# Kernel optimization log

Measured on AMD Instinct MI355X. Metric: run time of the kernel, lower is better.

Reference implementation:

```python
import jax, jax.numpy as jnp
import numpy as np

N_SPK = 8      # MAX_NO_OF_SPEAKERS
N_LAYERS = 2


def setup_inputs() -> dict:
    key = jax.random.key(0)
    B, S, H = 8, 1024, 512  # batch, seq_len, input_size==hidden_size==output_size
    k = jax.random.split(key, 6)
    x = jax.random.normal(k[0], (B, S, H), dtype=jnp.float32)
    speakers = jax.random.randint(k[1], (B, S), 0, N_SPK, dtype=jnp.int32)
    scale = 1.0 / np.sqrt(H).astype(np.float32)
    # per-speaker, per-layer GRU params (torch nn.GRU layout: gates [r,z,n])
    Wi = jax.random.uniform(k[2], (N_SPK, N_LAYERS, 3 * H, H), minval=-scale, maxval=scale, dtype=jnp.float32)
    Wh = jax.random.uniform(k[3], (N_SPK, N_LAYERS, 3 * H, H), minval=-scale, maxval=scale, dtype=jnp.float32)
    bi = jax.random.uniform(k[4], (N_SPK, N_LAYERS, 3 * H), minval=-scale, maxval=scale, dtype=jnp.float32)
    bh = jax.random.uniform(k[5], (N_SPK, N_LAYERS, 3 * H), minval=-scale, maxval=scale, dtype=jnp.float32)
    return {"x": x, "speakers": speakers, "Wi": Wi, "Wh": Wh, "bi": bi, "bh": bh}


def _gru_cell(x_t, h, Wi_l, Wh_l, bi_l, bh_l):
    # torch GRU cell: r,z,n gates
    gi = x_t @ Wi_l.T + bi_l          # [B, 3H]
    gh = h @ Wh_l.T + bh_l            # [B, 3H]
    ir, iz, i_n = jnp.split(gi, 3, axis=-1)
    hr, hz, h_n = jnp.split(gh, 3, axis=-1)
    r = jax.nn.sigmoid(ir + hr)
    z = jax.nn.sigmoid(iz + hz)
    n = jnp.tanh(i_n + r * h_n)
    return (1.0 - z) * n + z * h


def _forward(x, speakers, Wi, Wh, bi, bh):
    B, S, H = x.shape
    x_sb = jnp.swapaxes(x, 0, 1)              # [S, B, H]
    total = jnp.zeros((S, B, H), x.dtype)
    for sp in range(N_SPK):
        # masked-GRU equivalence: gathering speaker sp's utterances, running a
        # GRU, and scattering back == running over the full sequence while
        # freezing hidden state (and emitting 0) at non-sp timesteps.
        mask_sb = (speakers == sp).T          # [S, B]
        Wi_s, Wh_s, bi_s, bh_s = Wi[sp], Wh[sp], bi[sp], bh[sp]

        def step(h, xm):
            x_t, m_t = xm                     # [B,H], [B]
            m = m_t[:, None]
            inp = x_t
            new_h = []
            for l in range(N_LAYERS):
                hl = _gru_cell(inp, h[l], Wi_s[l], Wh_s[l], bi_s[l], bh_s[l])
                hl = jnp.where(m, hl, h[l])   # carry hidden across masked steps
                new_h.append(hl)
                inp = hl
            return jnp.stack(new_h), jnp.where(m, inp, 0.0)

        h0 = jnp.zeros((N_LAYERS, B, H), x.dtype)
        _, outs = jax.lax.scan(step, h0, (x_sb, mask_sb))  # outs: [S, B, H]
        total = total + outs                  # masks disjoint across speakers
    return jnp.swapaxes(total, 0, 1)          # [B, S, H]


def reference(x, speakers, Wi, Wh, bi, bh):
    return _forward(x, speakers, Wi, Wh, bi, bh)
```

## Files before the change

### kernel.cpp

```cpp
#include <hip/hip_runtime.h>
#include <cstdint>
#include <cstddef>

#define SS 1024
#define HH 512
#define G3 1536

typedef _Float16 half8 __attribute__((ext_vector_type(8)));
typedef float f32x4 __attribute__((ext_vector_type(4)));

static constexpr unsigned OFF_TLIST = 0;
static constexpr unsigned OFF_LEN   = 262144;
static constexpr unsigned OFF_META  = 262400;
static constexpr unsigned OFF_H0    = 262656;
static constexpr unsigned OFF_H1    = OFF_H0 + 131072;
static constexpr unsigned OFF_BAR   = OFF_H1 + 131072;
static constexpr unsigned WS_NEED   = OFF_BAR + 4096;

__device__ __forceinline__ half8 cvt8(const float* p) {
  float4 u = *(const float4*)p;
  float4 v = *(const float4*)(p + 4);
  half8 h;
  h[0]=(_Float16)u.x; h[1]=(_Float16)u.y; h[2]=(_Float16)u.z; h[3]=(_Float16)u.w;
  h[4]=(_Float16)v.x; h[5]=(_Float16)v.y; h[6]=(_Float16)v.z; h[7]=(_Float16)v.w;
  return h;
}

__device__ __forceinline__ float sigm(float x) { return 1.f / (1.f + __expf(-x)); }

__global__ void prep_kernel(const int* __restrict__ spk, int* __restrict__ tlist,
                            int* __restrict__ len, int* __restrict__ meta) {
  __shared__ int slen[64];
  const int t = threadIdx.x;
  const int sp = t >> 3, b = t & 7;
  int cnt = 0;
  int* tl = tlist + (sp * 8 + b) * SS;
  const int4* srow = (const int4*)(spk + b * SS);
#pragma unroll 4
  for (int i = 0; i < SS / 4; ++i) {
    int4 v = srow[i];
    if (v.x == sp) tl[cnt++] = 4 * i + 0;
    if (v.y == sp) tl[cnt++] = 4 * i + 1;
    if (v.z == sp) tl[cnt++] = 4 * i + 2;
    if (v.w == sp) tl[cnt++] = 4 * i + 3;
  }
  len[t] = cnt;
  slen[t] = cnt;
  for (int i = cnt; i < SS; ++i) tl[i] = 0;
  __syncthreads();
  if (t < 8) {
    int m = 0;
    for (int i = 0; i < 8; ++i) m = max(m, slen[t * 8 + i]);
    meta[t] = m;
  }
}

__launch_bounds__(256, 1)
__global__ void gru_main(const float* __restrict__ x,
                         const float* __restrict__ Wi, const float* __restrict__ Wh,
                         const float* __restrict__ bi, const float* __restrict__ bh,
                         const int* __restrict__ tlist, const int* __restrict__ len,
                         const int* __restrict__ meta,
                         unsigned short* __restrict__ h0ring,
                         unsigned short* __restrict__ h1ring,
                         float* __restrict__ out, unsigned* __restrict__ bar) {
  const int wg = blockIdx.x;
  const int sp = wg & 7;
  const int og = wg >> 3;
  const int j0 = og * 16;
  const int tid = threadIdx.x;
  const int w  = tid >> 6;
  const int l  = tid & 63;
  const int lr = l & 15;
  const int lg = l >> 4;
  const int b8 = lr & 7;

  __shared__ float accbuf[4][12][272];
  __shared__ _Float16 hstage[2][8][536];

  const size_t WMAT = (size_t)G3 * HH;
  const float* pWi0 = Wi + (size_t)(sp * 2 + 0) * WMAT;
  const float* pWh0 = Wh + (size_t)(sp * 2 + 0) * WMAT;
  const float* pWi1 = Wi + (size_t)(sp * 2 + 1) * WMAT;
  const float* pWh1 = Wh + (size_t)(sp * 2 + 1) * WMAT;

  half8 bwi0[3][4], bwh0[3][4], bwi1[3][4], bwh1[3][4];
#pragma unroll
  for (int T = 0; T < 3; ++T) {
#pragma unroll
    for (int q = 0; q < 4; ++q) {
      const size_t row = (size_t)(T * HH + j0 + lr);
      const int k0 = lg * 8 + (w * 4 + q) * 32;
      bwi0[T][q] = cvt8(pWi0 + row * HH + k0);
      bwh0[T][q] = cvt8(pWh0 + row * HH + k0);
      bwi1[T][q] = cvt8(pWi1 + row * HH + k0);
      bwh1[T][q] = cvt8(pWh1 + row * HH + k0);
    }
  }

  const bool isA = tid < 128;
  const int u_ = isA ? tid : (tid - 128);
  const int gb = u_ >> 4;
  const int gj = u_ & 15;
  const int Lb = len[sp * 8 + gb];
  const int* tlB = tlist + (sp * 8 + gb) * SS;
  float bAi[3], bAh[3], bBi[3], bBh[3];
#pragma unroll
  for (int g = 0; g < 3; ++g) {
    const int n = g * HH + j0 + gj;
    bAi[g] = bi[(sp * 2 + 0) * G3 + n];
    bAh[g] = bh[(sp * 2 + 0) * G3 + n];
    bBi[g] = bi[(sp * 2 + 1) * G3 + n];
    bBh[g] = bh[(sp * 2 + 1) * G3 + n];
  }

  const int* tlX = tlist + (sp * 8 + b8) * SS;
  const float* xrow_base = x + (size_t)b8 * SS * HH;

  const int maxlen = meta[sp];
  unsigned* flg = bar + sp * 32;

  float h0prev = 0.f, h1prev = 0.f;

  {
    const int tx = tlX[0];
    const float* xs = xrow_base + (size_t)tx * HH;
    half8 xf[4];
    f32x4 a0[3];
#pragma unroll
    for (int T = 0; T < 3; ++T)
#pragma unroll
      for (int e = 0; e < 4; ++e) a0[T][e] = 0.f;
#pragma unroll
    for (int q = 0; q < 4; ++q) xf[q] = cvt8(xs + lg * 8 + (w * 4 + q) * 32);
#pragma unroll
    for (int T = 0; T < 3; ++T)
#pragma unroll
      for (int q = 0; q < 4; ++q)
        a0[T] = __builtin_amdgcn_mfma_f32_16x16x32_f16(xf[q], bwi0[T][q], a0[T], 0, 0, 0);
#pragma unroll
    for (int T = 0; T < 3; ++T)
#pragma unroll
      for (int e = 0; e < 4; ++e)
        accbuf[w][T][(lg * 4 + e) * 17 + lr] = a0[T][e];
  }

  for (int r = 0; r <= maxlen; ++r) {
    {
      const int s0 = (r - 1) & 1;
      const int s1 = r & 1;
      const unsigned long long* src0 =
          (const unsigned long long*)(h0ring + ((size_t)(s0 * 64 + sp * 8)) * HH);
      const unsigned long long* src1 =
          (const unsigned long long*)(h1ring + ((size_t)(s1 * 64 + sp * 8)) * HH);
      unsigned long long v0[4], v1[4];
#pragma unroll
      for (int i = 0; i < 4; ++i) {
        const int e = i * 256 + tid;
        v0[i] = __hip_atomic_load(src0 + e, __ATOMIC_RELAXED, __HIP_MEMORY_SCOPE_AGENT);
        v1[i] = __hip_atomic_load(src1 + e, __ATOMIC_RELAXED, __HIP_MEMORY_SCOPE_AGENT);
      }
#pragma unroll
      for (int i = 0; i < 4; ++i) {
        const int e = i * 256 + tid;
        const int row = e >> 7;
        const int col = e & 127;
        *(unsigned long long*)((char*)&hstage[0][row][0] + col * 8) = v0[i];
        *(unsigned long long*)((char*)&hstage[1][row][0] + col * 8) = v1[i];
      }
    }
    __syncthreads();

    half8 hA0[4], hA1[4];
#pragma unroll
    for (int q = 0; q < 4; ++q) {
      const int k0 = lg * 8 + (w * 4 + q) * 32;
      hA0[q] = *(const half8*)((const char*)&hstage[0][b8][0] + k0 * 2);
      hA1[q] = *(const half8*)((const char*)&hstage[1][b8][0] + k0 * 2);
    }
    f32x4 acc[3][3];
#pragma unroll
    for (int Gm = 0; Gm < 3; ++Gm)
#pragma unroll
      for (int T = 0; T < 3; ++T)
#pragma unroll
        for (int e = 0; e < 4; ++e) acc[Gm][T][e] = 0.f;
#pragma unroll
    for (int T = 0; T < 3; ++T) {
#pragma unroll
      for (int q = 0; q < 4; ++q) {
        acc[0][T] = __builtin_amdgcn_mfma_f32_16x16x32_f16(hA0[q], bwh0[T][q], acc[0][T], 0, 0, 0);
        acc[1][T] = __builtin_amdgcn_mfma_f32_16x16x32_f16(hA0[q], bwi1[T][q], acc[1][T], 0, 0, 0);
        acc[2][T] = __builtin_amdgcn_mfma_f32_16x16x32_f16(hA1[q], bwh1[T][q], acc[2][T], 0, 0, 0);
      }
    }
#pragma unroll
    for (int Gm = 0; Gm < 3; ++Gm)
#pragma unroll
      for (int T = 0; T < 3; ++T)
#pragma unroll
        for (int e = 0; e < 4; ++e)
          accbuf[w][3 + Gm * 3 + T][(lg * 4 + e) * 17 + lr] = acc[Gm][T][e];
    __syncthreads();

    const bool actA = isA && (r < Lb);
    const bool actB = (!isA) && (r >= 1) && (r <= Lb);
    const int ci = gb * 17 + gj;
    if (actA) {
      float giv[3], ghv[3];
#pragma unroll
      for (int g = 0; g < 3; ++g) {
        giv[g] = accbuf[0][g][ci] + accbuf[1][g][ci] + accbuf[2][g][ci] + accbuf[3][g][ci] + bAi[g];
        ghv[g] = accbuf[0][3 + g][ci] + accbuf[1][3 + g][ci] + accbuf[2][3 + g][ci] + accbuf[3][3 + g][ci] + bAh[g];
      }
      const float rr = sigm(giv[0] + ghv[0]);
      const float zz = sigm(giv[1] + ghv[1]);
      const float nn = tanhf(giv[2] + rr * ghv[2]);
      const float hnew = (1.f - zz) * nn + zz * h0prev;
      h0prev = hnew;
      union { _Float16 h; unsigned short u; } cv; cv.h = (_Float16)hnew;
      __hip_atomic_store(&h0ring[((size_t)((r & 1) * 64 + sp * 8 + gb)) * HH + j0 + gj],
                         cv.u, __ATOMIC_RELAXED, __HIP_MEMORY_SCOPE_AGENT);
    } else if (actB) {
      float giv[3], ghv[3];
#pragma unroll
      for (int g = 0; g < 3; ++g) {
        giv[g] = accbuf[0][6 + g][ci] + accbuf[1][6 + g][ci] + accbuf[2][6 + g][ci] + accbuf[3][6 + g][ci] + bBi[g];
        ghv[g] = accbuf[0][9 + g][ci] + accbuf[1][9 + g][ci] + accbuf[2][9 + g][ci] + accbuf[3][9 + g][ci] + bBh[g];
      }
      const float rr = sigm(giv[0] + ghv[0]);
      const float zz = sigm(giv[1] + ghv[1]);
      const float nn = tanhf(giv[2] + rr * ghv[2]);
      const float hnew = (1.f - zz) * nn + zz * h1prev;
      h1prev = hnew;
      const int tcur = tlB[(r - 1) & (SS - 1)];
      union { _Float16 h; unsigned short u; } cv; cv.h = (_Float16)hnew;
      __hip_atomic_store(&h1ring[((size_t)(((r - 1) & 1) * 64 + sp * 8 + gb)) * HH + j0 + gj],
                         cv.u, __ATOMIC_RELAXED, __HIP_MEMORY_SCOPE_AGENT);
      out[((size_t)(gb * SS + tcur)) * HH + j0 + gj] = hnew;
    }

    __syncthreads();
    if (tid == 0)
      __hip_atomic_store(&flg[og], (unsigned)(r + 1), __ATOMIC_RELAXED, __HIP_MEMORY_SCOPE_AGENT);

    {
      const int tx = tlX[(r + 1) & (SS - 1)];
      const float* xs = xrow_base + (size_t)tx * HH;
      half8 xf[4];
      f32x4 a0[3];
#pragma unroll
      for (int T = 0; T < 3; ++T)
#pragma unroll
        for (int e = 0; e < 4; ++e) a0[T][e] = 0.f;
#pragma unroll
      for (int q = 0; q < 4; ++q) xf[q] = cvt8(xs + lg * 8 + (w * 4 + q) * 32);
#pragma unroll
      for (int T = 0; T < 3; ++T)
#pragma unroll
        for (int q = 0; q < 4; ++q)
          a0[T] = __builtin_amdgcn_mfma_f32_16x16x32_f16(xf[q], bwi0[T][q], a0[T], 0, 0, 0);
#pragma unroll
      for (int T = 0; T < 3; ++T)
#pragma unroll
        for (int e = 0; e < 4; ++e)
          accbuf[w][T][(lg * 4 + e) * 17 + lr] = a0[T][e];
    }

    if (tid < 64) {
      const unsigned tgt = (unsigned)(r + 1);
      const unsigned* f = flg + (tid & 31);
      unsigned iters = 0;
      while (__hip_atomic_load(f, __ATOMIC_RELAXED, __HIP_MEMORY_SCOPE_AGENT) < tgt) {
        __builtin_amdgcn_s_sleep(1);
        if (++iters > 100000000u) break;
      }
    }
    asm volatile("" ::: "memory");
    __syncthreads();
  }
}

extern "C" void kernel_launch(void* const* d_in, const int* in_sizes, int n_in,
                              void* d_out, int out_size, void* d_ws, size_t ws_size,
                              hipStream_t stream) {
  const float* x   = (const float*)d_in[0];
  const int*   spk = (const int*)d_in[1];
  const float* Wi  = (const float*)d_in[2];
  const float* Wh  = (const float*)d_in[3];
  const float* bi  = (const float*)d_in[4];
  const float* bh  = (const float*)d_in[5];
  float* out = (float*)d_out;
  char* ws = (char*)d_ws;

  int*            tlist = (int*)(ws + OFF_TLIST);
  int*            len   = (int*)(ws + OFF_LEN);
  int*            meta  = (int*)(ws + OFF_META);
  unsigned short* h0r   = (unsigned short*)(ws + OFF_H0);
  unsigned short* h1r   = (unsigned short*)(ws + OFF_H1);
  unsigned*       bar   = (unsigned*)(ws + OFF_BAR);

  (void)in_sizes; (void)n_in; (void)out_size; (void)ws_size;

  hipMemsetAsync(ws + OFF_H0, 0, WS_NEED - OFF_H0, stream);
  prep_kernel<<<1, 64, 0, stream>>>(spk, tlist, len, meta);
  gru_main<<<256, 256, 0, stream>>>(x, Wi, Wh, bi, bh, tlist, len, meta, h0r, h1r, out, bar);
}
```

Before: 661.5 us.

## Replace flag barrier with step-tagged hidden-state words polled by consumers

Each hidden-state element is now stored as a 32-bit word with the step number in the upper 16 bits, so consumers spin on the data itself instead of a separate per-speaker flag barrier. This removes the barrier round trip (flag store, poll, extra __syncthreads) from each recurrent step. Inactive steps now also write the carried value so tags stay current. It doubles ring traffic and uses a permute to unpack the fp16 halves. The accbuf layout is also changed to allow vectorized f32x4 stores.

After: 723.9 us. 9.4% more time.

```diff
diff --git a/kernel.cpp b/kernel.cpp
--- a/kernel.cpp
+++ b/kernel.cpp
@@ -13,9 +13,8 @@
 static constexpr unsigned OFF_LEN   = 262144;
 static constexpr unsigned OFF_META  = 262400;
 static constexpr unsigned OFF_H0    = 262656;
-static constexpr unsigned OFF_H1    = OFF_H0 + 131072;
-static constexpr unsigned OFF_BAR   = OFF_H1 + 131072;
-static constexpr unsigned WS_NEED   = OFF_BAR + 4096;
+static constexpr unsigned OFF_H1    = OFF_H0 + 262144;
+static constexpr unsigned WS_NEED   = OFF_H1 + 262144;
 
 __device__ __forceinline__ half8 cvt8(const float* p) {
   float4 u = *(const float4*)p;
@@ -24,6 +23,15 @@
   h[0]=(_Float16)u.x; h[1]=(_Float16)u.y; h[2]=(_Float16)u.z; h[3]=(_Float16)u.w;
   h[4]=(_Float16)v.x; h[5]=(_Float16)v.y; h[6]=(_Float16)v.z; h[7]=(_Float16)v.w;
   return h;
+}
+
+__device__ __forceinline__ half8 pack8(uint4 a, uint4 b) {
+  union { unsigned u[4]; half8 h; } r;
+  r.u[0] = __builtin_amdgcn_perm(a.y, a.x, 0x05040100);
+  r.u[1] = __builtin_amdgcn_perm(a.w, a.z, 0x05040100);
+  r.u[2] = __builtin_amdgcn_perm(b.y, b.x, 0x05040100);
+  r.u[3] = __builtin_amdgcn_perm(b.w, b.z, 0x05040100);
+  return r.h;
 }
 
 __device__ __forceinline__ float sigm(float x) { return 1.f / (1.f + __expf(-x)); }
@@ -61,9 +69,8 @@
                          const float* __restrict__ bi, const float* __restrict__ bh,
                          const int* __restrict__ tlist, const int* __restrict__ len,
                          const int* __restrict__ meta,
-                         unsigned short* __restrict__ h0ring,
-                         unsigned short* __restrict__ h1ring,
-                         float* __restrict__ out, unsigned* __restrict__ bar) {
+                         unsigned* __restrict__ h0ring, unsigned* __restrict__ h1ring,
+                         float* __restrict__ out) {
   const int wg = blockIdx.x;
   const int sp = wg & 7;
   const int og = wg >> 3;
@@ -75,8 +82,8 @@
   const int lg = l >> 4;
   const int b8 = lr & 7;
 
-  __shared__ float accbuf[4][12][272];
-  __shared__ _Float16 hstage[2][8][536];
+  __shared__ float accbuf[4][12][320];
+  __shared__ unsigned hstage[2][8][516];
 
   const size_t WMAT = (size_t)G3 * HH;
   const float* pWi0 = Wi + (size_t)(sp * 2 + 0) * WMAT;
@@ -118,7 +125,6 @@
   const float* xrow_base = x + (size_t)b8 * SS * HH;
 
   const int maxlen = meta[sp];
-  unsigned* flg = bar + sp * 32;
 
   float h0prev = 0.f, h1prev = 0.f;
 
@@ -140,33 +146,44 @@
         a0[T] = __builtin_amdgcn_mfma_f32_16x16x32_f16(xf[q], bwi0[T][q], a0[T], 0, 0, 0);
 #pragma unroll
     for (int T = 0; T < 3; ++T)
-#pragma unroll
-      for (int e = 0; e < 4; ++e)
-        accbuf[w][T][(lg * 4 + e) * 17 + lr] = a0[T][e];
+      *(f32x4*)&accbuf[w][T][lr * 20 + lg * 4] = a0[T];
   }
 
   for (int r = 0; r <= maxlen; ++r) {
     {
-      const int s0 = (r - 1) & 1;
-      const int s1 = r & 1;
-      const unsigned long long* src0 =
-          (const unsigned long long*)(h0ring + ((size_t)(s0 * 64 + sp * 8)) * HH);
-      const unsigned long long* src1 =
-          (const unsigned long long*)(h1ring + ((size_t)(s1 * 64 + sp * 8)) * HH);
-      unsigned long long v0[4], v1[4];
-#pragma unroll
-      for (int i = 0; i < 4; ++i) {
-        const int e = i * 256 + tid;
-        v0[i] = __hip_atomic_load(src0 + e, __ATOMIC_RELAXED, __HIP_MEMORY_SCOPE_AGENT);
-        v1[i] = __hip_atomic_load(src1 + e, __ATOMIC_RELAXED, __HIP_MEMORY_SCOPE_AGENT);
-      }
-#pragma unroll
-      for (int i = 0; i < 4; ++i) {
-        const int e = i * 256 + tid;
-        const int row = e >> 7;
-        const int col = e & 127;
-        *(unsigned long long*)((char*)&hstage[0][row][0] + col * 8) = v0[i];
-        *(unsigned long long*)((char*)&hstage[1][row][0] + col * 8) = v1[i];
+      const unsigned exp = (unsigned)r;
+      const unsigned* src0 = h0ring + ((size_t)(((r - 1) & 1) * 64 + sp * 8)) * HH;
+      const unsigned* src1 = h1ring + ((size_t)((r & 1) * 64 + sp * 8)) * HH;
+      unsigned v0[16], v1[16];
+#pragma unroll
+      for (int j = 0; j < 16; ++j) {
+        v0[j] = __hip_atomic_load(src0 + j * 256 + tid, __ATOMIC_RELAXED, __HIP_MEMORY_SCOPE_AGENT);
+        v1[j] = __hip_atomic_load(src1 + j * 256 + tid, __ATOMIC_RELAXED, __HIP_MEMORY_SCOPE_AGENT);
+      }
+      unsigned iters = 0;
+      while (true) {
+        unsigned bad = 0;
+#pragma unroll
+        for (int j = 0; j < 16; ++j) {
+          bad |= (v0[j] >> 16) ^ exp;
+          bad |= (v1[j] >> 16) ^ exp;
+        }
+        if (!bad) break;
+        __builtin_amdgcn_s_sleep(1);
+        if (++iters > 100000000u) break;
+#pragma unroll
+        for (int j = 0; j < 16; ++j) {
+          if ((v0[j] >> 16) != exp)
+            v0[j] = __hip_atomic_load(src0 + j * 256 + tid, __ATOMIC_RELAXED, __HIP_MEMORY_SCOPE_AGENT);
+          if ((v1[j] >> 16) != exp)
+            v1[j] = __hip_atomic_load(src1 + j * 256 + tid, __ATOMIC_RELAXED, __HIP_MEMORY_SCOPE_AGENT);
+        }
+      }
+#pragma unroll
+      for (int j = 0; j < 16; ++j) {
+        const int e = j * 256 + tid;
+        hstage[0][e >> 9][e & 511] = v0[j];
+        hstage[1][e >> 9][e & 511] = v1[j];
       }
     }
     __syncthreads();
@@ -175,8 +192,12 @@
 #pragma unroll
     for (int q = 0; q < 4; ++q) {
       const int k0 = lg * 8 + (w * 4 + q) * 32;
-      hA0[q] = *(const half8*)((const char*)&hstage[0][b8][0] + k0 * 2);
-      hA1[q] = *(const half8*)((const char*)&hstage[1][b8][0] + k0 * 2);
+      uint4 a0 = *(const uint4*)&hstage[0][b8][k0];
+      uint4 a1 = *(const uint4*)&hstage[0][b8][k0 + 4];
+      uint4 c0 = *(const uint4*)&hstage[1][b8][k0];
+      uint4 c1 = *(const uint4*)&hstage[1][b8][k0 + 4];
+      hA0[q] = pack8(a0, a1);
+      hA1[q] = pack8(c0, c1);
     }
     f32x4 acc[3][3];
 #pragma unroll
@@ -198,51 +219,48 @@
     for (int Gm = 0; Gm < 3; ++Gm)
 #pragma unroll
       for (int T = 0; T < 3; ++T)
-#pragma unroll
-        for (int e = 0; e < 4; ++e)
-          accbuf[w][3 + Gm * 3 + T][(lg * 4 + e) * 17 + lr] = acc[Gm][T][e];
+        *(f32x4*)&accbuf[w][3 + Gm * 3 + T][lr * 20 + lg * 4] = acc[Gm][T];
     __syncthreads();
 
-    const bool actA = isA && (r < Lb);
-    const bool actB = (!isA) && (r >= 1) && (r <= Lb);
-    const int ci = gb * 17 + gj;
-    if (actA) {
-      float giv[3], ghv[3];
-#pragma unroll
-      for (int g = 0; g < 3; ++g) {
-        giv[g] = accbuf[0][g][ci] + accbuf[1][g][ci] + accbuf[2][g][ci] + accbuf[3][g][ci] + bAi[g];
-        ghv[g] = accbuf[0][3 + g][ci] + accbuf[1][3 + g][ci] + accbuf[2][3 + g][ci] + accbuf[3][3 + g][ci] + bAh[g];
-      }
-      const float rr = sigm(giv[0] + ghv[0]);
-      const float zz = sigm(giv[1] + ghv[1]);
-      const float nn = tanhf(giv[2] + rr * ghv[2]);
-      const float hnew = (1.f - zz) * nn + zz * h0prev;
-      h0prev = hnew;
-      union { _Float16 h; unsigned short u; } cv; cv.h = (_Float16)hnew;
+    const int ci = gj * 20 + gb;
+    const unsigned tagw = ((unsigned)(r + 1)) << 16;
+    if (isA) {
+      if (r < Lb) {
+        float giv[3], ghv[3];
+#pragma unroll
+        for (int g = 0; g < 3; ++g) {
+          giv[g] = accbuf[0][g][ci] + accbuf[1][g][ci] + accbuf[2][g][ci] + accbuf[3][g][ci] + bAi[g];
+          ghv[g] = accbuf[0][3 + g][ci] + accbuf[1][3 + g][ci] + accbuf[2][3 + g][ci] + accbuf[3][3 + g][ci] + bAh[g];
+        }
+        const float rr = sigm(giv[0] + ghv[0]);
+        const float zz = sigm(giv[1] + ghv[1]);
+        const float nn = tanhf(giv[2] + rr * ghv[2]);
+        h0prev = (1.f - zz) * nn + zz * h0prev;
+      }
+      union { _Float16 hf; unsigned short us; } cv; cv.hf = (_Float16)h0prev;
       __hip_atomic_store(&h0ring[((size_t)((r & 1) * 64 + sp * 8 + gb)) * HH + j0 + gj],
-                         cv.u, __ATOMIC_RELAXED, __HIP_MEMORY_SCOPE_AGENT);
-    } else if (actB) {
-      float giv[3], ghv[3];
-#pragma unroll
-      for (int g = 0; g < 3; ++g) {
-        giv[g] = accbuf[0][6 + g][ci] + accbuf[1][6 + g][ci] + accbuf[2][6 + g][ci] + accbuf[3][6 + g][ci] + bBi[g];
-        ghv[g] = accbuf[0][9 + g][ci] + accbuf[1][9 + g][ci] + accbuf[2][9 + g][ci] + accbuf[3][9 + g][ci] + bBh[g];
-      }
-      const float rr = sigm(giv[0] + ghv[0]);
-      const float zz = sigm(giv[1] + ghv[1]);
-      const float nn = tanhf(giv[2] + rr * ghv[2]);
-      const float hnew = (1.f - zz) * nn + zz * h1prev;
-      h1prev = hnew;
-      const int tcur = tlB[(r - 1) & (SS - 1)];
-      union { _Float16 h; unsigned short u; } cv; cv.h = (_Float16)hnew;
+                         tagw | (unsigned)cv.us, __ATOMIC_RELAXED, __HIP_MEMORY_SCOPE_AGENT);
+    } else {
+      if ((r >= 1) && (r <= Lb)) {
+        float giv[3], ghv[3];
+#pragma unroll
+        for (int g = 0; g < 3; ++g) {
+          giv[g] = accbuf[0][6 + g][ci] + accbuf[1][6 + g][ci] + accbuf[2][6 + g][ci] + accbuf[3][6 + g][ci] + bBi[g];
+          ghv[g] = accbuf[0][9 + g][ci] + accbuf[1][9 + g][ci] + accbuf[2][9 + g][ci] + accbuf[3][9 + g][ci] + bBh[g];
+        }
+        const float rr = sigm(giv[0] + ghv[0]);
+        const float zz = sigm(giv[1] + ghv[1]);
+        const float nn = tanhf(giv[2] + rr * ghv[2]);
+        h1prev = (1.f - zz) * nn + zz * h1prev;
+        const int tcur = tlB[(r - 1) & (SS - 1)];
+        out[((size_t)(gb * SS + tcur)) * HH + j0 + gj] = h1prev;
+      }
+      union { _Float16 hf; unsigned short us; } cv; cv.hf = (_Float16)h1prev;
       __hip_atomic_store(&h1ring[((size_t)(((r - 1) & 1) * 64 + sp * 8 + gb)) * HH + j0 + gj],
-                         cv.u, __ATOMIC_RELAXED, __HIP_MEMORY_SCOPE_AGENT);
-      out[((size_t)(gb * SS + tcur)) * HH + j0 + gj] = hnew;
+                         tagw | (unsigned)cv.us, __ATOMIC_RELAXED, __HIP_MEMORY_SCOPE_AGENT);
     }
 
     __syncthreads();
-    if (tid == 0)
-      __hip_atomic_store(&flg[og], (unsigned)(r + 1), __ATOMIC_RELAXED, __HIP_MEMORY_SCOPE_AGENT);
 
     {
       const int tx = tlX[(r + 1) & (SS - 1)];
@@ -262,22 +280,8 @@
           a0[T] = __builtin_amdgcn_mfma_f32_16x16x32_f16(xf[q], bwi0[T][q], a0[T], 0, 0, 0);
 #pragma unroll
       for (int T = 0; T < 3; ++T)
-#pragma unroll
-        for (int e = 0; e < 4; ++e)
-          accbuf[w][T][(lg * 4 + e) * 17 + lr] = a0[T][e];
-    }
-
-    if (tid < 64) {
-      const unsigned tgt = (unsigned)(r + 1);
-      const unsigned* f = flg + (tid & 31);
-      unsigned iters = 0;
-      while (__hip_atomic_load(f, __ATOMIC_RELAXED, __HIP_MEMORY_SCOPE_AGENT) < tgt) {
-        __builtin_amdgcn_s_sleep(1);
-        if (++iters > 100000000u) break;
-      }
-    }
-    asm volatile("" ::: "memory");
-    __syncthreads();
+        *(f32x4*)&accbuf[w][T][lr * 20 + lg * 4] = a0[T];
+    }
   }
 }
 
@@ -293,16 +297,15 @@
   float* out = (float*)d_out;
   char* ws = (char*)d_ws;
 
-  int*            tlist = (int*)(ws + OFF_TLIST);
-  int*            len   = (int*)(ws + OFF_LEN);
-  int*            meta  = (int*)(ws + OFF_META);
-  unsigned short* h0r   = (unsigned short*)(ws + OFF_H0);
-  unsigned short* h1r   = (unsigned short*)(ws + OFF_H1);
-  unsigned*       bar   = (unsigned*)(ws + OFF_BAR);
+  int*      tlist = (int*)(ws + OFF_TLIST);
+  int*      len   = (int*)(ws + OFF_LEN);
+  int*      meta  = (int*)(ws + OFF_META);
+  unsigned* h0r   = (unsigned*)(ws + OFF_H0);
+  unsigned* h1r   = (unsigned*)(ws + OFF_H1);
 
   (void)in_sizes; (void)n_in; (void)out_size; (void)ws_size;
 
   hipMemsetAsync(ws + OFF_H0, 0, WS_NEED - OFF_H0, stream);
   prep_kernel<<<1, 64, 0, stream>>>(spk, tlist, len, meta);
-  gru_main<<<256, 256, 0, stream>>>(x, Wi, Wh, bi, bh, tlist, len, meta, h0r, h1r, out, bar);
-}
+  gru_main<<<256, 256, 0, stream>>>(x, Wi, Wh, bi, bh, tlist, len, meta, h0r, h1r, out);
+}
```
